# Optimization experiments

Hardware: AMD Instinct MI355X
Metric: run time of the kernel (lower is better)

Reference implementation:

```python
import jax, jax.numpy as jnp
import numpy as np

LAMBDA_DECAY = 0.01   # self.lambda_decay
ALPHA = 0.95          # self.alpha_continuity
TAU = 0.0             # self.tau
LN_EPS = 1e-5

M, D = 8192, 4096


def layer_norm(x):
    m = jnp.mean(x, axis=-1, keepdims=True)
    v = jnp.var(x, axis=-1, keepdims=True)
    return (x - m) / jnp.sqrt(v + LN_EPS)


def setup_inputs() -> dict:
    key = jax.random.key(0)
    k1, k2, k3, k4, k5 = jax.random.split(key, 5)
    return {
        "states": jax.random.normal(k1, (M, D), dtype=jnp.float32),       # memory bank cell states
        "weights": jax.random.uniform(k2, (M,), dtype=jnp.float32),        # per-cell weights
        "timestamps": jax.random.uniform(k3, (M,), dtype=jnp.float32),     # per-cell timestamps
        "current_state": jax.random.normal(k4, (D,), dtype=jnp.float32),
        "sensed_state": jax.random.normal(k5, (D,), dtype=jnp.float32),    # appended to bank; not in output math
        "t_new": jnp.ones((1,), dtype=jnp.float32),
    }


def reference(states, weights, timestamps, current_state, sensed_state, t_new):
    # Batched per-cell decay update (replaces the Python loop with .item() syncs):
    # cell.weight *= exp(-lambda * |(t_new - cell.timestamp) - tau|)
    decay = jnp.exp(-LAMBDA_DECAY * jnp.abs((t_new[0] - timestamps) - TAU))  # [M]
    w = weights * decay                                                       # [M]

    # scaled_dot single-query attention over the memory bank, modulated by cell weights
    scale = 1.0 / jnp.sqrt(jnp.asarray(states.shape[-1], dtype=states.dtype))
    scores = (states @ current_state) * scale        # [M]
    attn = jax.nn.softmax(scores)                    # [M]
    wa = attn * w
    wa = wa / (jnp.sum(wa) + 1e-9)                   # renormalize by decayed cell weights
    attention_out = wa @ states                      # [D]

    # recursive update: new = alpha * current + (1 - alpha) * attention_out
    new_state = ALPHA * current_state + (1.0 - ALPHA) * attention_out

    # layer norm of the new persistent state
    return layer_norm(new_state)
```

## Files before the change

kernel.cpp:

```cpp
#include <hip/hip_runtime.h>
#include <math.h>

#define LAMBDA_DECAY 0.01f
#define ALPHA 0.95f
#define LN_EPS 1e-5f

#define WPB 4
#define RPW 4
#define NPART 512
#define G2 64
#define NP2 8

static __device__ __forceinline__ float wave_sum_all(float v) {
#pragma unroll
    for (int o = 32; o > 0; o >>= 1) v += __shfl_xor(v, o);
    return v;
}

static __device__ float block_sum(float v, float* sh, int nwaves) {
    int lane = threadIdx.x & 63;
    int w = threadIdx.x >> 6;
    v = wave_sum_all(v);
    if (lane == 0) sh[w] = v;
    __syncthreads();
    float r = 0.0f;
    for (int i = 0; i < nwaves; ++i) r += sh[i];
    __syncthreads();
    return r;
}

__global__ __launch_bounds__(256, 2) void fused_kernel(
    const float* __restrict__ states, const float* __restrict__ cur,
    const float* __restrict__ weights, const float* __restrict__ ts,
    const float* __restrict__ t_new,
    float* __restrict__ partial, float* __restrict__ partE, float* __restrict__ partS,
    int M, int D, float scale)
{
    __shared__ float4 lds4[1024];
    __shared__ float shE[WPB], shS[WPB];

    const int wid = threadIdx.x >> 6;
    const int lane = threadIdx.x & 63;
    const int r0 = (blockIdx.x * WPB + wid) * RPW;

    const float4* c4 = (const float4*)cur;
    float4 curv[16];
#pragma unroll
    for (int j = 0; j < 16; ++j) curv[j] = c4[j * 64 + lane];

    float4 acc[16];
#pragma unroll
    for (int j = 0; j < 16; ++j) acc[j] = make_float4(0.f, 0.f, 0.f, 0.f);

    float E = 0.0f, S = 0.0f;
    const float tn = t_new[0];

    for (int rr = 0; rr < RPW; ++rr) {
        const int row = r0 + rr;
        if (row >= M) break;
        const float4* rp = (const float4*)(states + (size_t)row * D);
        float4 rv[16];
#pragma unroll
        for (int j = 0; j < 16; ++j) rv[j] = rp[j * 64 + lane];

        float s = 0.0f;
#pragma unroll
        for (int j = 0; j < 16; ++j) {
            s = fmaf(rv[j].x, curv[j].x, s);
            s = fmaf(rv[j].y, curv[j].y, s);
            s = fmaf(rv[j].z, curv[j].z, s);
            s = fmaf(rv[j].w, curv[j].w, s);
        }
        s = wave_sum_all(s);

        const float e = expf(s * scale);
        const float w = weights[row] * expf(-LAMBDA_DECAY * fabsf(tn - ts[row]));
        const float p = e * w;
        E += e; S += p;

#pragma unroll
        for (int j = 0; j < 16; ++j) {
            acc[j].x = fmaf(p, rv[j].x, acc[j].x);
            acc[j].y = fmaf(p, rv[j].y, acc[j].y);
            acc[j].z = fmaf(p, rv[j].z, acc[j].z);
            acc[j].w = fmaf(p, rv[j].w, acc[j].w);
        }
    }

    if (wid == 0) {
#pragma unroll
        for (int j = 0; j < 16; ++j) lds4[j * 64 + lane] = acc[j];
        if (lane == 0) { shE[0] = E; shS[0] = S; }
    }
    __syncthreads();
    for (int w = 1; w < WPB; ++w) {
        if (wid == w) {
#pragma unroll
            for (int j = 0; j < 16; ++j) {
                float4 t = lds4[j * 64 + lane];
                t.x += acc[j].x; t.y += acc[j].y; t.z += acc[j].z; t.w += acc[j].w;
                lds4[j * 64 + lane] = t;
            }
            if (lane == 0) { shE[w] = E; shS[w] = S; }
        }
        __syncthreads();
    }

    float4* pb = (float4*)(partial + (size_t)blockIdx.x * D);
#pragma unroll
    for (int jj = 0; jj < 4; ++jj)
        pb[jj * 256 + threadIdx.x] = lds4[jj * 256 + threadIdx.x];
    if (threadIdx.x == 0) {
        float e = 0.f, sp = 0.f;
        for (int w = 0; w < WPB; ++w) { e += shE[w]; sp += shS[w]; }
        partE[blockIdx.x] = e;
        partS[blockIdx.x] = sp;
    }
}

__global__ __launch_bounds__(256) void reduce_kernel(
    const float* __restrict__ partial, float* __restrict__ partial2, int D)
{
    const int col = blockIdx.x * 256 + threadIdx.x;
    const int b0 = blockIdx.y * G2;
    float a = 0.0f;
    for (int b = 0; b < G2; ++b)
        a += partial[(size_t)(b0 + b) * D + col];
    partial2[(size_t)blockIdx.y * D + col] = a;
}

__global__ __launch_bounds__(1024) void finalize_kernel(
    const float* __restrict__ partial2, const float* __restrict__ partE,
    const float* __restrict__ partS, const float* __restrict__ cur,
    float* __restrict__ out, int D)
{
    __shared__ float sh[16];
    const int tid = threadIdx.x;

    float E = 0.0f, S = 0.0f;
    for (int i = tid; i < NPART; i += 1024) { E += partE[i]; S += partS[i]; }
    E = block_sum(E, sh, 16);
    S = block_sum(S, sh, 16);
    const float inv = 1.0f / (S + 1e-9f * E);

    float v[4];
    float s = 0.0f, s2 = 0.0f;
#pragma unroll
    for (int k = 0; k < 4; ++k) {
        const int c = tid + k * 1024;
        float a = 0.0f;
#pragma unroll
        for (int y = 0; y < NP2; ++y) a += partial2[y * D + c];
        const float nv = ALPHA * cur[c] + (1.0f - ALPHA) * (a * inv);
        v[k] = nv;
        s += nv; s2 += nv * nv;
    }
    s = block_sum(s, sh, 16);
    s2 = block_sum(s2, sh, 16);
    const float mean = s / (float)D;
    const float var = s2 / (float)D - mean * mean;
    const float rstd = 1.0f / sqrtf(var + LN_EPS);
#pragma unroll
    for (int k = 0; k < 4; ++k)
        out[tid + k * 1024] = (v[k] - mean) * rstd;
}

extern "C" void kernel_launch(void* const* d_in, const int* in_sizes, int n_in,
                              void* d_out, int out_size, void* d_ws, size_t ws_size,
                              hipStream_t stream) {
    const float* states     = (const float*)d_in[0];
    const float* weights    = (const float*)d_in[1];
    const float* timestamps = (const float*)d_in[2];
    const float* current    = (const float*)d_in[3];
    const float* t_new      = (const float*)d_in[5];
    float* out = (float*)d_out;

    const int M = in_sizes[1];
    const int D = in_sizes[3];

    float* ws       = (float*)d_ws;
    float* partial  = ws;
    float* partial2 = partial + (size_t)NPART * D;
    float* partE    = partial2 + (size_t)NP2 * D;
    float* partS    = partE + NPART;

    const float scale = 1.0f / sqrtf((float)D);

    fused_kernel<<<NPART, 256, 0, stream>>>(
        states, current, weights, timestamps, t_new,
        partial, partE, partS, M, D, scale);

    {
        dim3 grid(D / 256, NP2);
        reduce_kernel<<<grid, 256, 0, stream>>>(partial, partial2, D);
    }

    finalize_kernel<<<1, 1024, 0, stream>>>(partial2, partE, partS, current, out, D);
}
```

Measured before the change: 41.31 us.

## Double-buffer row loads, stage query vector in LDS, use nontemporal loads

The main kernel now prefetches the next row into a second register buffer while computing the current one, using nontemporal loads for the streamed states. The query vector moves from 64 registers per thread into shared memory to free registers. The dot product is split into four independent accumulators, and the reduce kernel uses two accumulators. The goal is to hide memory latency in a bandwidth-bound pass, at the cost of extra LDS reads per row and more registers for the double buffer. The row-bounds check is also removed, so the kernel assumes M divides evenly.

```diff
diff --git a/kernel.cpp b/kernel.cpp
--- a/kernel.cpp
+++ b/kernel.cpp
@@ -10,6 +10,8 @@
 #define NPART 512
 #define G2 64
 #define NP2 8
+
+typedef float v4f __attribute__((ext_vector_type(4)));
 
 static __device__ __forceinline__ float wave_sum_all(float v) {
 #pragma unroll
@@ -36,42 +38,60 @@
     float* __restrict__ partial, float* __restrict__ partE, float* __restrict__ partS,
     int M, int D, float scale)
 {
-    __shared__ float4 lds4[1024];
+    __shared__ v4f shbuf[1024];
     __shared__ float shE[WPB], shS[WPB];
 
     const int wid = threadIdx.x >> 6;
     const int lane = threadIdx.x & 63;
     const int r0 = (blockIdx.x * WPB + wid) * RPW;
 
-    const float4* c4 = (const float4*)cur;
-    float4 curv[16];
-#pragma unroll
-    for (int j = 0; j < 16; ++j) curv[j] = c4[j * 64 + lane];
-
-    float4 acc[16];
-#pragma unroll
-    for (int j = 0; j < 16; ++j) acc[j] = make_float4(0.f, 0.f, 0.f, 0.f);
+    const v4f* c4 = (const v4f*)cur;
+#pragma unroll
+    for (int j = 0; j < 4; ++j)
+        shbuf[j * 256 + threadIdx.x] = c4[j * 256 + threadIdx.x];
+    __syncthreads();
+
+    v4f acc[16];
+#pragma unroll
+    for (int j = 0; j < 16; ++j) acc[j] = (v4f)(0.0f);
 
     float E = 0.0f, S = 0.0f;
     const float tn = t_new[0];
 
+    v4f rv[2][16];
+    {
+        const v4f* rp = (const v4f*)(states + (size_t)r0 * D);
+#pragma unroll
+        for (int j = 0; j < 16; ++j)
+            rv[0][j] = __builtin_nontemporal_load(&rp[j * 64 + lane]);
+    }
+
+#pragma unroll
     for (int rr = 0; rr < RPW; ++rr) {
         const int row = r0 + rr;
-        if (row >= M) break;
-        const float4* rp = (const float4*)(states + (size_t)row * D);
-        float4 rv[16];
-#pragma unroll
-        for (int j = 0; j < 16; ++j) rv[j] = rp[j * 64 + lane];
-
-        float s = 0.0f;
-#pragma unroll
-        for (int j = 0; j < 16; ++j) {
-            s = fmaf(rv[j].x, curv[j].x, s);
-            s = fmaf(rv[j].y, curv[j].y, s);
-            s = fmaf(rv[j].z, curv[j].z, s);
-            s = fmaf(rv[j].w, curv[j].w, s);
+        const int cb = rr & 1;
+        const int nb = cb ^ 1;
+
+        if (rr + 1 < RPW) {
+            const v4f* rp = (const v4f*)(states + (size_t)(row + 1) * D);
+#pragma unroll
+            for (int j = 0; j < 16; ++j)
+                rv[nb][j] = __builtin_nontemporal_load(&rp[j * 64 + lane]);
         }
-        s = wave_sum_all(s);
+
+        float s0 = 0.f, s1 = 0.f, s2 = 0.f, s3 = 0.f;
+#pragma unroll
+        for (int j = 0; j < 16; j += 4) {
+            v4f a0 = rv[cb][j + 0], c0 = shbuf[(j + 0) * 64 + lane];
+            v4f a1 = rv[cb][j + 1], c1 = shbuf[(j + 1) * 64 + lane];
+            v4f a2 = rv[cb][j + 2], c2 = shbuf[(j + 2) * 64 + lane];
+            v4f a3 = rv[cb][j + 3], c3 = shbuf[(j + 3) * 64 + lane];
+            s0 = fmaf(a0[0], c0[0], fmaf(a0[1], c0[1], fmaf(a0[2], c0[2], fmaf(a0[3], c0[3], s0))));
+            s1 = fmaf(a1[0], c1[0], fmaf(a1[1], c1[1], fmaf(a1[2], c1[2], fmaf(a1[3], c1[3], s1))));
+            s2 = fmaf(a2[0], c2[0], fmaf(a2[1], c2[1], fmaf(a2[2], c2[2], fmaf(a2[3], c2[3], s2))));
+            s3 = fmaf(a3[0], c3[0], fmaf(a3[1], c3[1], fmaf(a3[2], c3[2], fmaf(a3[3], c3[3], s3))));
+        }
+        float s = wave_sum_all((s0 + s1) + (s2 + s3));
 
         const float e = expf(s * scale);
         const float w = weights[row] * expf(-LAMBDA_DECAY * fabsf(tn - ts[row]));
@@ -79,37 +99,31 @@
         E += e; S += p;
 
 #pragma unroll
-        for (int j = 0; j < 16; ++j) {
-            acc[j].x = fmaf(p, rv[j].x, acc[j].x);
-            acc[j].y = fmaf(p, rv[j].y, acc[j].y);
-            acc[j].z = fmaf(p, rv[j].z, acc[j].z);
-            acc[j].w = fmaf(p, rv[j].w, acc[j].w);
-        }
-    }
-
+        for (int j = 0; j < 16; ++j)
+            acc[j] += p * rv[cb][j];
+    }
+
+    __syncthreads();
     if (wid == 0) {
 #pragma unroll
-        for (int j = 0; j < 16; ++j) lds4[j * 64 + lane] = acc[j];
+        for (int j = 0; j < 16; ++j) shbuf[j * 64 + lane] = acc[j];
         if (lane == 0) { shE[0] = E; shS[0] = S; }
     }
     __syncthreads();
     for (int w = 1; w < WPB; ++w) {
         if (wid == w) {
 #pragma unroll
-            for (int j = 0; j < 16; ++j) {
-                float4 t = lds4[j * 64 + lane];
-                t.x += acc[j].x; t.y += acc[j].y; t.z += acc[j].z; t.w += acc[j].w;
-                lds4[j * 64 + lane] = t;
-            }
+            for (int j = 0; j < 16; ++j)
+                shbuf[j * 64 + lane] += acc[j];
             if (lane == 0) { shE[w] = E; shS[w] = S; }
         }
         __syncthreads();
     }
 
-    float4* pb = (float4*)(partial + (size_t)blockIdx.x * D);
+    v4f* pb = (v4f*)(partial + (size_t)blockIdx.x * D);
 #pragma unroll
     for (int jj = 0; jj < 4; ++jj)
-        pb[jj * 256 + threadIdx.x] = lds4[jj * 256 + threadIdx.x];
+        pb[jj * 256 + threadIdx.x] = shbuf[jj * 256 + threadIdx.x];
     if (threadIdx.x == 0) {
         float e = 0.f, sp = 0.f;
         for (int w = 0; w < WPB; ++w) { e += shE[w]; sp += shS[w]; }
@@ -123,10 +137,12 @@
 {
     const int col = blockIdx.x * 256 + threadIdx.x;
     const int b0 = blockIdx.y * G2;
-    float a = 0.0f;
-    for (int b = 0; b < G2; ++b)
-        a += partial[(size_t)(b0 + b) * D + col];
-    partial2[(size_t)blockIdx.y * D + col] = a;
+    float a0 = 0.0f, a1 = 0.0f;
+    for (int b = 0; b < G2; b += 2) {
+        a0 += partial[(size_t)(b0 + b) * D + col];
+        a1 += partial[(size_t)(b0 + b + 1) * D + col];
+    }
+    partial2[(size_t)blockIdx.y * D + col] = a0 + a1;
 }
 
 __global__ __launch_bounds__(1024) void finalize_kernel(
```

Measured after the change: 48.10 us. 1.16x slower.
